# Performance work log

Hardware: AMD Instinct MI355X
Metric: run time of the kernel (lower is better)

Reference implementation:

```python
import jax, jax.numpy as jnp
import numpy as np

B = 8192          # batch
D = 256           # feature_dim
H = 64            # num attention heads
HD = D // H       # head_dim = 4
NC, NB, NF, NT = 2048, 2048, 512, 768
NCLS = 26
EPS = 1e-5


def _linear_params(k, out_d, in_d):
    s = 1.0 / np.sqrt(in_d)
    kw, kb = jax.random.split(k)
    W = jax.random.uniform(kw, (out_d, in_d), minval=-s, maxval=s, dtype=jnp.float32)
    b = jax.random.uniform(kb, (out_d,), minval=-s, maxval=s, dtype=jnp.float32)
    return W, b


def setup_inputs() -> dict:
    key = jax.random.key(0)
    ks = jax.random.split(key, 16)
    inp = {
        'x_context': jax.random.normal(ks[0], (B, NC), dtype=jnp.float32),
        'x_body':    jax.random.normal(ks[1], (B, NB), dtype=jnp.float32),
        'x_face':    jax.random.normal(ks[2], (B, NF), dtype=jnp.float32),
        'x_text':    jax.random.normal(ks[3], (B, NT), dtype=jnp.float32),
    }
    inp['Wc'], inp['bc'] = _linear_params(ks[4], D, NC)
    inp['Wb'], inp['bb'] = _linear_params(ks[5], D, NB)
    inp['Wf'], inp['bf'] = _linear_params(ks[6], D, NF)
    inp['Wt'], inp['bt'] = _linear_params(ks[7], D, NT)
    # MultiheadAttention packed in-proj (3D x D) and out-proj
    inp['in_w'], inp['in_b'] = _linear_params(ks[8], 3 * D, D)
    inp['out_w'], inp['out_b'] = _linear_params(ks[9], D, D)
    # gate MLP
    inp['Wg1'], inp['bg1'] = _linear_params(ks[10], D, D)
    inp['Wg2'], inp['bg2'] = _linear_params(ks[11], 1, D)
    # fusion head
    inp['W1'], inp['b1'] = _linear_params(ks[12], D, 4 * D)
    inp['gamma'] = jnp.ones((D,), dtype=jnp.float32)
    inp['beta'] = jnp.zeros((D,), dtype=jnp.float32)
    inp['W2'], inp['b2'] = _linear_params(ks[13], NCLS, D)
    return inp


def reference(x_context, x_body, x_face, x_text,
              Wc, bc, Wb, bb, Wf, bf, Wt, bt,
              in_w, in_b, out_w, out_b,
              Wg1, bg1, Wg2, bg2,
              W1, b1, gamma, beta, W2, b2):
    # per-modality projections -> [B, 4, D]
    f = jnp.stack([
        x_context @ Wc.T + bc,
        x_body    @ Wb.T + bb,
        x_face    @ Wf.T + bf,
        x_text    @ Wt.T + bt,
    ], axis=1)
    bsz = f.shape[0]

    # MultiheadAttention with seq_len=1 per token: softmax over a single key
    Wq, Wk, Wv = jnp.split(in_w, 3, axis=0)
    bq, bk, bv = jnp.split(in_b, 3)
    q = (f @ Wq.T + bq).reshape(bsz, 4, H, HD)
    k = (f @ Wk.T + bk).reshape(bsz, 4, H, HD)
    v = (f @ Wv.T + bv).reshape(bsz, 4, H, HD)
    scores = jnp.sum(q * k, axis=-1, keepdims=True) / np.sqrt(HD)  # [B,4,H,1]
    w = jax.nn.softmax(scores, axis=-1)                            # == 1 (single key)
    attn = (w * v).reshape(bsz, 4, D)
    self_out = attn @ out_w.T + out_b                              # [B,4,D]

    # cross attention: with seq_len=1 the output depends only on key/value,
    # so each (query i, key 3-j) call equals the self-style output of modality 3-j;
    # combining over the 4 key variants reduces to the mean over modalities.
    cross = jnp.mean(self_out, axis=1, keepdims=True)              # [B,1,D]

    gate = jax.nn.sigmoid(jax.nn.relu(self_out @ Wg1.T + bg1) @ Wg2.T + bg2)  # [B,4,1]
    combined = gate * self_out + (1.0 - gate) * cross              # [B,4,D]

    h = combined.reshape(bsz, 4 * D) @ W1.T + b1                   # [B,D]
    # BatchNorm1d (training-mode batch statistics, biased variance)
    mu = jnp.mean(h, axis=0)
    var = jnp.var(h, axis=0)
    h = (h - mu) / jnp.sqrt(var + EPS) * gamma + beta
    h = jax.nn.relu(h)                                             # dropout = identity (eval)
    return h @ W2.T + b2                                           # [B,26]
```

## Files before the change

kernel.cpp:

```cpp
#include <hip/hip_runtime.h>
#include <math.h>

typedef __attribute__((ext_vector_type(8))) short bf16x8;
typedef __attribute__((ext_vector_type(4))) float f32x4;
typedef unsigned short u16;
typedef unsigned int u32;

#define BSZ   8192
#define BN_EPS 1e-5f

__device__ inline u16 f2bf(float x) {
    u32 u = __float_as_uint(x);
    u32 r = (u + 0x7FFFu + ((u >> 16) & 1u)) >> 16;
    return (u16)r;
}
__device__ inline float bf2f_lo(u32 p) { return __uint_as_float(p << 16); }
__device__ inline float bf2f_hi(u32 p) { return __uint_as_float(p & 0xFFFF0000u); }

__device__ inline void async_g2l(const void* g, void* l) {
    __builtin_amdgcn_global_load_lds(
        (const __attribute__((address_space(1))) void*)g,
        (__attribute__((address_space(3))) void*)l, 16, 0, 0);
}

__global__ __launch_bounds__(256)
void wvo_kernel(const float* __restrict__ in_w, const float* __restrict__ in_b,
                const float* __restrict__ out_w, const float* __restrict__ out_b,
                float* __restrict__ wvo, float* __restrict__ bvo)
{
    const int i = blockIdx.x;
    const int j = threadIdx.x;
    const float* Wv = in_w + 512 * 256;
    float s = 0.f;
    for (int k = 0; k < 256; ++k)
        s = fmaf(out_w[i * 256 + k], Wv[k * 256 + j], s);
    wvo[i * 256 + j] = s;
    if (i == 0) {
        const float* bv = in_b + 512;
        float t = 0.f;
        for (int k = 0; k < 256; ++k)
            t = fmaf(out_w[j * 256 + k], bv[k], t);
        bvo[j] = t + out_b[j];
    }
}

__global__ __launch_bounds__(256)
void cvt_weights(const float* __restrict__ wvo, const float* __restrict__ Wc,
                 const float* __restrict__ Wb,  const float* __restrict__ Wf,
                 const float* __restrict__ Wt,  const float* __restrict__ Wg1,
                 const float* __restrict__ W1f, u16* __restrict__ dst)
{
    int gid = blockIdx.x * 256 + threadIdx.x;
    const float* src; u16* d; int loc;
    if      (gid <   8192) { src = wvo; d = dst + 0;       loc = gid; }
    else if (gid <  73728) { src = Wc;  d = dst + 65536;   loc = gid - 8192; }
    else if (gid < 139264) { src = Wb;  d = dst + 589824;  loc = gid - 73728; }
    else if (gid < 155648) { src = Wf;  d = dst + 1114112; loc = gid - 139264; }
    else if (gid < 180224) { src = Wt;  d = dst + 1245184; loc = gid - 155648; }
    else if (gid < 188416) { src = Wg1; d = dst + 1441792; loc = gid - 180224; }
    else                   { src = W1f; d = dst + 1507328; loc = gid - 188416; }
    const float4 v0 = *(const float4*)(src + (size_t)loc * 8);
    const float4 v1 = *(const float4*)(src + (size_t)loc * 8 + 4);
    uint4 o;
    o.x = (u32)f2bf(v0.x) | ((u32)f2bf(v0.y) << 16);
    o.y = (u32)f2bf(v0.z) | ((u32)f2bf(v0.w) << 16);
    o.z = (u32)f2bf(v1.x) | ((u32)f2bf(v1.y) << 16);
    o.w = (u32)f2bf(v1.z) | ((u32)f2bf(v1.w) << 16);
    *(uint4*)(d + (size_t)loc * 8) = o;
}

template<int ASRC, int EPI>
__device__ void gemm_core(const void* Ap, const u16* __restrict__ Wp,
                          const float* __restrict__ bias,
                          u16* __restrict__ outb, float* __restrict__ outf,
                          const float* __restrict__ wg2, float* __restrict__ gpart,
                          int K, int RMUL, int ROFF, int bm)
{
    __shared__ u16 As[64 * 64];
    __shared__ u16 Bs[256 * 64];
    const int t = threadIdx.x;
    const int w = t >> 6, l = t & 63;

    f32x4 acc[4][4];
    const f32x4 z = {0.f, 0.f, 0.f, 0.f};
#pragma unroll
    for (int i = 0; i < 4; ++i)
#pragma unroll
        for (int j = 0; j < 4; ++j) acc[i][j] = z;

    for (int k0 = 0; k0 < K; k0 += 64) {
#pragma unroll
        for (int it = 0; it < 8; ++it) {
            const int n  = it * 32 + w * 8 + (l >> 3);
            const int ch = (l & 7) ^ (n & 7);
            async_g2l(Wp + (size_t)n * K + k0 + ch * 8, Bs + it * 2048 + w * 512);
        }
        if (ASRC == 0) {
            const u16* Ab = (const u16*)Ap;
#pragma unroll
            for (int it = 0; it < 2; ++it) {
                const int row = it * 32 + w * 8 + (l >> 3);
                const int ch  = (l & 7) ^ (row & 7);
                async_g2l(Ab + (size_t)(bm + row) * K + k0 + ch * 8,
                          As + it * 2048 + w * 512);
            }
        } else {
            const float* Af = (const float*)Ap;
            const int row = t >> 2, kq = t & 3;
            const float* g = Af + (size_t)(bm + row) * K + k0 + kq * 16;
            const float4 v0 = *(const float4*)(g + 0);
            const float4 v1 = *(const float4*)(g + 4);
            const float4 v2 = *(const float4*)(g + 8);
            const float4 v3 = *(const float4*)(g + 12);
            bf16x8 p0, p1;
            p0[0] = (short)f2bf(v0.x); p0[1] = (short)f2bf(v0.y);
            p0[2] = (short)f2bf(v0.z); p0[3] = (short)f2bf(v0.w);
            p0[4] = (short)f2bf(v1.x); p0[5] = (short)f2bf(v1.y);
            p0[6] = (short)f2bf(v1.z); p0[7] = (short)f2bf(v1.w);
            p1[0] = (short)f2bf(v2.x); p1[1] = (short)f2bf(v2.y);
            p1[2] = (short)f2bf(v2.z); p1[3] = (short)f2bf(v2.w);
            p1[4] = (short)f2bf(v3.x); p1[5] = (short)f2bf(v3.y);
            p1[6] = (short)f2bf(v3.z); p1[7] = (short)f2bf(v3.w);
            char* ab = (char*)As;
            *(bf16x8*)(ab + row * 128 + (((kq * 2 + 0) ^ (row & 7)) << 4)) = p0;
            *(bf16x8*)(ab + row * 128 + (((kq * 2 + 1) ^ (row & 7)) << 4)) = p1;
        }
        __syncthreads();
        const char* ab = (const char*)As;
        const char* bb = (const char*)Bs;
#pragma unroll
        for (int kk = 0; kk < 2; ++kk) {
            bf16x8 af[4], bq[4];
#pragma unroll
            for (int i = 0; i < 4; ++i) {
                const int row = i * 16 + (l & 15);
                const int ch  = (l >> 4) + kk * 4;
                af[i] = *(const bf16x8*)(ab + row * 128 + ((ch ^ (row & 7)) << 4));
            }
#pragma unroll
            for (int j = 0; j < 4; ++j) {
                const int n  = w * 64 + j * 16 + (l & 15);
                const int ch = (l >> 4) + kk * 4;
                bq[j] = *(const bf16x8*)(bb + n * 128 + ((ch ^ (n & 7)) << 4));
            }
#pragma unroll
            for (int i = 0; i < 4; ++i)
#pragma unroll
                for (int j = 0; j < 4; ++j)
                    acc[i][j] = __builtin_amdgcn_mfma_f32_16x16x32_bf16(
                        af[i], bq[j], acc[i][j], 0, 0, 0);
        }
        __syncthreads();
    }

    if (EPI == 2) {
        float s[4][4];
#pragma unroll
        for (int i = 0; i < 4; ++i)
#pragma unroll
            for (int r = 0; r < 4; ++r) s[i][r] = 0.f;
#pragma unroll
        for (int j = 0; j < 4; ++j) {
            const int col = w * 64 + j * 16 + (l & 15);
            const float bv = bias[col], wv = wg2[col];
#pragma unroll
            for (int i = 0; i < 4; ++i)
#pragma unroll
                for (int r = 0; r < 4; ++r)
                    s[i][r] += fmaxf(acc[i][j][r] + bv, 0.f) * wv;
        }
#pragma unroll
        for (int off = 1; off < 16; off <<= 1)
#pragma unroll
            for (int i = 0; i < 4; ++i)
#pragma unroll
                for (int r = 0; r < 4; ++r)
                    s[i][r] += __shfl_xor(s[i][r], off);
        if ((l & 15) == 0) {
#pragma unroll
            for (int i = 0; i < 4; ++i)
#pragma unroll
                for (int r = 0; r < 4; ++r)
                    gpart[(size_t)w * 32768 + bm + i * 16 + ((l >> 4) << 2) + r] = s[i][r];
        }
    } else {
#pragma unroll
        for (int j = 0; j < 4; ++j) {
            const int col = w * 64 + j * 16 + (l & 15);
            const float bv = bias[col];
#pragma unroll
            for (int i = 0; i < 4; ++i) {
#pragma unroll
                for (int r = 0; r < 4; ++r) {
                    const int rt = i * 16 + ((l >> 4) << 2) + r;
                    const float v = acc[i][j][r] + bv;
                    const size_t orow = (size_t)(bm + rt) * RMUL + ROFF;
                    if (EPI == 0) outb[orow * 256 + col] = f2bf(v);
                    else          outf[orow * 256 + col] = v;
                }
            }
        }
    }
}

template<int ASRC, int EPI>
__global__ __launch_bounds__(256)
void gemm_k(const void* Ap, const u16* __restrict__ Wp, const float* __restrict__ bias,
            u16* __restrict__ outb, float* __restrict__ outf,
            const float* __restrict__ wg2, float* __restrict__ gpart, int K)
{
    gemm_core<ASRC, EPI>(Ap, Wp, bias, outb, outf, wg2, gpart, K, 1, 0, blockIdx.x * 64);
}

__global__ __launch_bounds__(256)
void gemm_proj(const float* A0, const float* A1, const float* A2, const float* A3,
               const u16* Wp0, const u16* Wp1, const u16* Wp2, const u16* Wp3,
               const float* b0, const float* b1, const float* b2, const float* b3,
               u16* __restrict__ fb)
{
    const int m = blockIdx.y;
    const float* A = (m == 0) ? A0 : (m == 1) ? A1 : (m == 2) ? A2 : A3;
    const u16* W   = (m == 0) ? Wp0 : (m == 1) ? Wp1 : (m == 2) ? Wp2 : Wp3;
    const float* b = (m == 0) ? b0 : (m == 1) ? b1 : (m == 2) ? b2 : b3;
    const int K    = (m == 0) ? 2048 : (m == 1) ? 2048 : (m == 2) ? 512 : 768;
    gemm_core<1, 0>(A, W, b, fb, nullptr, nullptr, nullptr, K, 4, m, blockIdx.x * 64);
}

__global__ __launch_bounds__(256)
void gate_fin(const float* __restrict__ gp, const float* __restrict__ bg2,
              float* __restrict__ gate)
{
    const int r = blockIdx.x * 256 + threadIdx.x;
    const float v = gp[r] + gp[32768 + r] + gp[65536 + r] + gp[98304 + r] + bg2[0];
    gate[r] = 1.f / (1.f + expf(-v));
}

__global__ __launch_bounds__(256)
void combined_k(const u16* __restrict__ so, const float* __restrict__ gate,
                u16* __restrict__ comb)
{
    const int idx = blockIdx.x * 256 + threadIdx.x;
    const int b = idx >> 7, p = idx & 127;
    const u32* s32 = (const u32*)so;
    u32* c32 = (u32*)comb;
    float lo[4], hi[4], gv[4];
#pragma unroll
    for (int m = 0; m < 4; ++m) {
        const u32 pk = s32[(size_t)(b * 4 + m) * 128 + p];
        lo[m] = bf2f_lo(pk); hi[m] = bf2f_hi(pk);
        gv[m] = gate[b * 4 + m];
    }
    const float cl = 0.25f * (lo[0] + lo[1] + lo[2] + lo[3]);
    const float ch = 0.25f * (hi[0] + hi[1] + hi[2] + hi[3]);
#pragma unroll
    for (int m = 0; m < 4; ++m) {
        const float ol = gv[m] * lo[m] + (1.f - gv[m]) * cl;
        const float oh = gv[m] * hi[m] + (1.f - gv[m]) * ch;
        c32[(size_t)b * 512 + m * 128 + p] = (u32)f2bf(ol) | ((u32)f2bf(oh) << 16);
    }
}

__global__ __launch_bounds__(256)
void bn_part(const float* __restrict__ h, float* __restrict__ psum,
             float* __restrict__ psq)
{
    const int p = blockIdx.x;
    const int d = threadIdx.x;
    float s = 0.f, q = 0.f;
    for (int r = 0; r < 128; ++r) {
        const float v = h[((size_t)p * 128 + r) * 256 + d];
        s += v;
        q = fmaf(v, v, q);
    }
    psum[p * 256 + d] = s;
    psq[p * 256 + d]  = q;
}

__global__ __launch_bounds__(256)
void bn_fin(const float* __restrict__ psum, const float* __restrict__ psq,
            const float* __restrict__ gamma, const float* __restrict__ beta,
            float* __restrict__ scale, float* __restrict__ shift)
{
    const int d = threadIdx.x;
    float s = 0.f, q = 0.f;
    for (int p = 0; p < 64; ++p) { s += psum[p * 256 + d]; q += psq[p * 256 + d]; }
    const float mu  = s * (1.f / BSZ);
    const float var = q * (1.f / BSZ) - mu * mu;
    const float inv = rsqrtf(var + BN_EPS);
    const float sc  = gamma[d] * inv;
    scale[d] = sc;
    shift[d] = beta[d] - mu * sc;
}

__global__ __launch_bounds__(256)
void final_kernel(const float* __restrict__ h, const float* __restrict__ scale,
                  const float* __restrict__ shift, const float* __restrict__ W2,
                  const float* __restrict__ b2, float* __restrict__ out)
{
    __shared__ float W2s[26][260];
    __shared__ float scs[256], shs[256];
    const int t = threadIdx.x;
    for (int u = t; u < 26 * 256; u += 256) {
        const int c = u >> 8, n = u & 255;
        W2s[c][(n >> 6) * 65 + (n & 63)] = W2[u];
    }
    scs[t] = scale[t];
    shs[t] = shift[t];
    __syncthreads();

    const int r = blockIdx.x * 64 + (t >> 2);
    const int p = t & 3;
    float acc[26];
#pragma unroll
    for (int c = 0; c < 26; ++c) acc[c] = 0.f;
    const float* hr = h + (size_t)r * 256 + p * 64;
#pragma unroll 4
    for (int i = 0; i < 64; ++i) {
        const int n = p * 64 + i;
        const float v = fmaxf(fmaf(hr[i], scs[n], shs[n]), 0.f);
        const int sw = p * 65 + i;
#pragma unroll
        for (int c = 0; c < 26; ++c)
            acc[c] = fmaf(v, W2s[c][sw], acc[c]);
    }
#pragma unroll
    for (int off = 1; off < 4; off <<= 1)
#pragma unroll
        for (int c = 0; c < 26; ++c)
            acc[c] += __shfl_xor(acc[c], off);
    if (p == 0) {
#pragma unroll
        for (int c = 0; c < 26; ++c)
            out[(size_t)r * 26 + c] = acc[c] + b2[c];
    }
}

extern "C" void kernel_launch(void* const* d_in, const int* in_sizes, int n_in,
                              void* d_out, int out_size, void* d_ws, size_t ws_size,
                              hipStream_t stream)
{
    const float* x_ctx  = (const float*)d_in[0];
    const float* x_body = (const float*)d_in[1];
    const float* x_face = (const float*)d_in[2];
    const float* x_text = (const float*)d_in[3];
    const float* Wc = (const float*)d_in[4];  const float* bc = (const float*)d_in[5];
    const float* Wb = (const float*)d_in[6];  const float* bb = (const float*)d_in[7];
    const float* Wf = (const float*)d_in[8];  const float* bf = (const float*)d_in[9];
    const float* Wt = (const float*)d_in[10]; const float* bt = (const float*)d_in[11];
    const float* in_w  = (const float*)d_in[12]; const float* in_b  = (const float*)d_in[13];
    const float* out_w = (const float*)d_in[14]; const float* out_b = (const float*)d_in[15];
    const float* Wg1 = (const float*)d_in[16]; const float* bg1 = (const float*)d_in[17];
    const float* Wg2 = (const float*)d_in[18]; const float* bg2 = (const float*)d_in[19];
    const float* W1  = (const float*)d_in[20]; const float* b1  = (const float*)d_in[21];
    const float* gamma = (const float*)d_in[22]; const float* beta = (const float*)d_in[23];
    const float* W2  = (const float*)d_in[24]; const float* b2  = (const float*)d_in[25];

    char* wsb = (char*)d_ws;
    u16*   f_bf  = (u16*)(wsb + 0);
    u16*   comb  = f_bf;
    u16*   so_bf = (u16*)(wsb + (16u << 20));
    float* h     = (float*)(wsb + (16u << 20));
    u16*   wpb   = (u16*)(wsb + (32u << 20));
    float* wvo   = (float*)(wsb + (36u << 20));
    float* bvo   = (float*)(wsb + (36u << 20) + 262144);
    float* gpart = (float*)(wsb + (37u << 20));
    float* gate  = (float*)(wsb + (38u << 20));
    float* psum  = (float*)(wsb + (39u << 20));
    float* psq   = (float*)(wsb + (39u << 20) + 65536);
    float* scale = (float*)(wsb + (39u << 20) + 131072);
    float* shift = (float*)(wsb + (39u << 20) + 135168);

    u16* wvo_bf = wpb + 0;
    u16* wc_bf  = wpb + 65536;
    u16* wb_bf  = wpb + 589824;
    u16* wf_bf  = wpb + 1114112;
    u16* wt_bf  = wpb + 1245184;
    u16* wg1_bf = wpb + 1441792;
    u16* w1_bf  = wpb + 1507328;

    wvo_kernel<<<256, 256, 0, stream>>>(in_w, in_b, out_w, out_b, wvo, bvo);
    cvt_weights<<<864, 256, 0, stream>>>(wvo, Wc, Wb, Wf, Wt, Wg1, W1, wpb);

    gemm_proj<<<dim3(128, 4), 256, 0, stream>>>(x_ctx, x_body, x_face, x_text,
                                                wc_bf, wb_bf, wf_bf, wt_bf,
                                                bc, bb, bf, bt, f_bf);

    gemm_k<0, 0><<<512, 256, 0, stream>>>(f_bf, wvo_bf, bvo, so_bf, nullptr,
                                          nullptr, nullptr, 256);

    gemm_k<0, 2><<<512, 256, 0, stream>>>(so_bf, wg1_bf, bg1, nullptr, nullptr,
                                          Wg2, gpart, 256);
    gate_fin<<<128, 256, 0, stream>>>(gpart, bg2, gate);

    combined_k<<<4096, 256, 0, stream>>>(so_bf, gate, comb);

    gemm_k<0, 1><<<128, 256, 0, stream>>>(comb, w1_bf, b1, nullptr, h,
                                          nullptr, nullptr, 1024);

    bn_part<<<64, 256, 0, stream>>>(h, psum, psq);
    bn_fin<<<1, 256, 0, stream>>>(psum, psq, gamma, beta, scale, shift);
    final_kernel<<<128, 256, 0, stream>>>(h, scale, shift, W2, b2, (float*)d_out);
}
```

Before: 166.1 us.

## Fuse self-out, gate MLP, combine and W1 GEMMs into one kernel; double-buffer projection GEMM

```diff
diff --git a/kernel.cpp b/kernel.cpp
--- a/kernel.cpp
+++ b/kernel.cpp
@@ -32,6 +32,7 @@
     const int j = threadIdx.x;
     const float* Wv = in_w + 512 * 256;
     float s = 0.f;
+#pragma unroll 8
     for (int k = 0; k < 256; ++k)
         s = fmaf(out_w[i * 256 + k], Wv[k * 256 + j], s);
     wvo[i * 256 + j] = s;
@@ -69,79 +70,90 @@
     *(uint4*)(d + (size_t)loc * 8) = o;
 }
 
-template<int ASRC, int EPI>
-__device__ void gemm_core(const void* Ap, const u16* __restrict__ Wp,
-                          const float* __restrict__ bias,
-                          u16* __restrict__ outb, float* __restrict__ outf,
-                          const float* __restrict__ wg2, float* __restrict__ gpart,
-                          int K, int RMUL, int ROFF, int bm)
-{
-    __shared__ u16 As[64 * 64];
-    __shared__ u16 Bs[256 * 64];
+__global__ __launch_bounds__(256)
+void gemm_proj(const float* __restrict__ A0, const float* __restrict__ A1,
+               const float* __restrict__ A2, const float* __restrict__ A3,
+               const u16* __restrict__ Wp0, const u16* __restrict__ Wp1,
+               const u16* __restrict__ Wp2, const u16* __restrict__ Wp3,
+               const float* __restrict__ b0, const float* __restrict__ b1,
+               const float* __restrict__ b2, const float* __restrict__ b3,
+               u16* __restrict__ fb)
+{
+    __shared__ u16 As[2][4096];
+    __shared__ u16 Bs[2][16384];
+    const int m = blockIdx.y;
+    const float* A  = (m == 0) ? A0 : (m == 1) ? A1 : (m == 2) ? A2 : A3;
+    const u16* Wp   = (m == 0) ? Wp0 : (m == 1) ? Wp1 : (m == 2) ? Wp2 : Wp3;
+    const float* bi = (m == 0) ? b0 : (m == 1) ? b1 : (m == 2) ? b2 : b3;
+    const int K     = (m == 0) ? 2048 : (m == 1) ? 2048 : (m == 2) ? 512 : 768;
+    const int nt = K >> 6;
+
     const int t = threadIdx.x;
     const int w = t >> 6, l = t & 63;
-
-    f32x4 acc[4][4];
-    const f32x4 z = {0.f, 0.f, 0.f, 0.f};
-#pragma unroll
-    for (int i = 0; i < 4; ++i)
-#pragma unroll
-        for (int j = 0; j < 4; ++j) acc[i][j] = z;
-
-    for (int k0 = 0; k0 < K; k0 += 64) {
+    const int bm = blockIdx.x * 64;
+    const int arow = t >> 2, akq = t & 3;
+
+    float4 ar[4];
+    auto loadA = [&](int k0) {
+        const float* g = A + (size_t)(bm + arow) * K + k0 + akq * 16;
+        ar[0] = *(const float4*)(g + 0);
+        ar[1] = *(const float4*)(g + 4);
+        ar[2] = *(const float4*)(g + 8);
+        ar[3] = *(const float4*)(g + 12);
+    };
+    auto writeA = [&](int buf) {
+        bf16x8 p0, p1;
+        p0[0] = (short)f2bf(ar[0].x); p0[1] = (short)f2bf(ar[0].y);
+        p0[2] = (short)f2bf(ar[0].z); p0[3] = (short)f2bf(ar[0].w);
+        p0[4] = (short)f2bf(ar[1].x); p0[5] = (short)f2bf(ar[1].y);
+        p0[6] = (short)f2bf(ar[1].z); p0[7] = (short)f2bf(ar[1].w);
+        p1[0] = (short)f2bf(ar[2].x); p1[1] = (short)f2bf(ar[2].y);
+        p1[2] = (short)f2bf(ar[2].z); p1[3] = (short)f2bf(ar[2].w);
+        p1[4] = (short)f2bf(ar[3].x); p1[5] = (short)f2bf(ar[3].y);
+        p1[6] = (short)f2bf(ar[3].z); p1[7] = (short)f2bf(ar[3].w);
+        char* abw = (char*)As[buf];
+        *(bf16x8*)(abw + arow * 128 + (((akq * 2 + 0) ^ (arow & 7)) << 4)) = p0;
+        *(bf16x8*)(abw + arow * 128 + (((akq * 2 + 1) ^ (arow & 7)) << 4)) = p1;
+    };
+    auto issueB = [&](int k0, int buf) {
 #pragma unroll
         for (int it = 0; it < 8; ++it) {
             const int n  = it * 32 + w * 8 + (l >> 3);
             const int ch = (l & 7) ^ (n & 7);
-            async_g2l(Wp + (size_t)n * K + k0 + ch * 8, Bs + it * 2048 + w * 512);
-        }
-        if (ASRC == 0) {
-            const u16* Ab = (const u16*)Ap;
-#pragma unroll
-            for (int it = 0; it < 2; ++it) {
-                const int row = it * 32 + w * 8 + (l >> 3);
-                const int ch  = (l & 7) ^ (row & 7);
-                async_g2l(Ab + (size_t)(bm + row) * K + k0 + ch * 8,
-                          As + it * 2048 + w * 512);
-            }
-        } else {
-            const float* Af = (const float*)Ap;
-            const int row = t >> 2, kq = t & 3;
-            const float* g = Af + (size_t)(bm + row) * K + k0 + kq * 16;
-            const float4 v0 = *(const float4*)(g + 0);
-            const float4 v1 = *(const float4*)(g + 4);
-            const float4 v2 = *(const float4*)(g + 8);
-            const float4 v3 = *(const float4*)(g + 12);
-            bf16x8 p0, p1;
-            p0[0] = (short)f2bf(v0.x); p0[1] = (short)f2bf(v0.y);
-            p0[2] = (short)f2bf(v0.z); p0[3] = (short)f2bf(v0.w);
-            p0[4] = (short)f2bf(v1.x); p0[5] = (short)f2bf(v1.y);
-            p0[6] = (short)f2bf(v1.z); p0[7] = (short)f2bf(v1.w);
-            p1[0] = (short)f2bf(v2.x); p1[1] = (short)f2bf(v2.y);
-            p1[2] = (short)f2bf(v2.z); p1[3] = (short)f2bf(v2.w);
-            p1[4] = (short)f2bf(v3.x); p1[5] = (short)f2bf(v3.y);
-            p1[6] = (short)f2bf(v3.z); p1[7] = (short)f2bf(v3.w);
-            char* ab = (char*)As;
-            *(bf16x8*)(ab + row * 128 + (((kq * 2 + 0) ^ (row & 7)) << 4)) = p0;
-            *(bf16x8*)(ab + row * 128 + (((kq * 2 + 1) ^ (row & 7)) << 4)) = p1;
-        }
-        __syncthreads();
-        const char* ab = (const char*)As;
-        const char* bb = (const char*)Bs;
+            async_g2l(Wp + (size_t)n * K + k0 + ch * 8, Bs[buf] + it * 2048 + w * 512);
+        }
+    };
+
+    f32x4 acc[4][4];
+    const f32x4 z = {0.f, 0.f, 0.f, 0.f};
+#pragma unroll
+    for (int i = 0; i < 4; ++i)
+#pragma unroll
+        for (int j = 0; j < 4; ++j) acc[i][j] = z;
+
+    loadA(0);
+    issueB(0, 0);
+    writeA(0);
+    __syncthreads();
+
+    for (int t0 = 0; t0 < nt; ++t0) {
+        const int cur = t0 & 1;
+        if (t0 + 1 < nt) { loadA((t0 + 1) * 64); issueB((t0 + 1) * 64, cur ^ 1); }
+        const char* abr = (const char*)As[cur];
+        const char* bbr = (const char*)Bs[cur];
 #pragma unroll
         for (int kk = 0; kk < 2; ++kk) {
             bf16x8 af[4], bq[4];
+            const int ch = kk * 4 + (l >> 4);
 #pragma unroll
             for (int i = 0; i < 4; ++i) {
-                const int row = i * 16 + (l & 15);
-                const int ch  = (l >> 4) + kk * 4;
-                af[i] = *(const bf16x8*)(ab + row * 128 + ((ch ^ (row & 7)) << 4));
+                const int fr = i * 16 + (l & 15);
+                af[i] = *(const bf16x8*)(abr + fr * 128 + ((ch ^ (fr & 7)) << 4));
             }
 #pragma unroll
             for (int j = 0; j < 4; ++j) {
-                const int n  = w * 64 + j * 16 + (l & 15);
-                const int ch = (l >> 4) + kk * 4;
-                bq[j] = *(const bf16x8*)(bb + n * 128 + ((ch ^ (n & 7)) << 4));
+                const int n = w * 64 + j * 16 + (l & 15);
+                bq[j] = *(const bf16x8*)(bbr + n * 128 + ((ch ^ (n & 7)) << 4));
             }
 #pragma unroll
             for (int i = 0; i < 4; ++i)
@@ -150,10 +162,157 @@
                     acc[i][j] = __builtin_amdgcn_mfma_f32_16x16x32_bf16(
                         af[i], bq[j], acc[i][j], 0, 0, 0);
         }
-        __syncthreads();
-    }
-
-    if (EPI == 2) {
+        if (t0 + 1 < nt) writeA(cur ^ 1);
+        __syncthreads();
+    }
+
+#pragma unroll
+    for (int j = 0; j < 4; ++j) {
+        const int col = w * 64 + j * 16 + (l & 15);
+        const float bv = bi[col];
+#pragma unroll
+        for (int i = 0; i < 4; ++i)
+#pragma unroll
+            for (int r = 0; r < 4; ++r) {
+                const int rt = i * 16 + ((l >> 4) << 2) + r;
+                fb[((size_t)(bm + rt) * 4 + m) * 256 + col] = f2bf(acc[i][j][r] + bv);
+            }
+    }
+}
+
+__global__ __launch_bounds__(256)
+void fused_mid(const u16* __restrict__ fb, const u16* __restrict__ wvo_bf,
+               const float* __restrict__ bvo,
+               const u16* __restrict__ wg1_bf, const float* __restrict__ bg1,
+               const float* __restrict__ wg2, const float* __restrict__ bg2,
+               const u16* __restrict__ w1_bf, const float* __restrict__ b1p,
+               float* __restrict__ h)
+{
+    __shared__ u16 AS[16384];
+    __shared__ u16 BS[16384];
+    __shared__ float gp[4][64];
+    __shared__ float gate[64];
+    const int t = threadIdx.x, w = t >> 6, l = t & 63;
+    const int bm = blockIdx.x * 64;
+    char* const ab = (char*)AS;
+    char* const bb = (char*)BS;
+
+    float4 br[8];
+    auto loadB = [&](const u16* Wp, int K, int k0) {
+#pragma unroll
+        for (int it = 0; it < 8; ++it) {
+            const int n  = it * 32 + w * 8 + (l >> 3);
+            const int ch = (l & 7) ^ (n & 7);
+            br[it] = *(const float4*)(Wp + (size_t)n * K + k0 + ch * 8);
+        }
+    };
+    auto writeB = [&]() {
+#pragma unroll
+        for (int it = 0; it < 8; ++it)
+            *(float4*)(bb + it * 4096 + w * 1024 + l * 16) = br[it];
+    };
+
+#pragma unroll
+    for (int it = 0; it < 8; ++it) {
+        const int r  = it * 8 + w * 2 + (l >> 5);
+        const int ch = l & 31;
+        async_g2l(fb + (size_t)(bm + r) * 256 + ((ch ^ (r & 7)) << 3),
+                  AS + it * 2048 + w * 512);
+    }
+    loadB(wvo_bf, 256, 0);
+    __syncthreads();
+
+    const f32x4 z = {0.f, 0.f, 0.f, 0.f};
+
+    f32x4 acc[4][4];
+#pragma unroll
+    for (int i = 0; i < 4; ++i)
+#pragma unroll
+        for (int j = 0; j < 4; ++j) acc[i][j] = z;
+
+    for (int it4 = 0; it4 < 4; ++it4) {
+        __syncthreads();
+        writeB();
+        if (it4 < 3) loadB(wvo_bf, 256, (it4 + 1) * 64);
+        __syncthreads();
+#pragma unroll
+        for (int kk = 0; kk < 2; ++kk) {
+            const int ks  = it4 * 2 + kk;
+            const int chB = kk * 4 + (l >> 4);
+            bf16x8 af[4], bq[4];
+#pragma unroll
+            for (int i = 0; i < 4; ++i) {
+                const int fr = i * 16 + (l & 15);
+                af[i] = *(const bf16x8*)(ab + fr * 512 +
+                          (((ks * 4 + (l >> 4)) ^ (fr & 7)) << 4));
+            }
+#pragma unroll
+            for (int j = 0; j < 4; ++j) {
+                const int n = w * 64 + j * 16 + (l & 15);
+                bq[j] = *(const bf16x8*)(bb + n * 128 + ((chB ^ (n & 7)) << 4));
+            }
+#pragma unroll
+            for (int i = 0; i < 4; ++i)
+#pragma unroll
+                for (int j = 0; j < 4; ++j)
+                    acc[i][j] = __builtin_amdgcn_mfma_f32_16x16x32_bf16(
+                        af[i], bq[j], acc[i][j], 0, 0, 0);
+        }
+    }
+
+    loadB(wg1_bf, 256, 0);
+    __syncthreads();
+#pragma unroll
+    for (int j = 0; j < 4; ++j) {
+        const int col = w * 64 + j * 16 + (l & 15);
+        const float bv = bvo[col];
+#pragma unroll
+        for (int i = 0; i < 4; ++i)
+#pragma unroll
+            for (int r = 0; r < 4; ++r) {
+                const int rt = i * 16 + ((l >> 4) << 2) + r;
+                *(u16*)(ab + rt * 512 + (((col >> 3) ^ (rt & 7)) << 4) + (col & 7) * 2)
+                    = f2bf(acc[i][j][r] + bv);
+            }
+    }
+
+    f32x4 g2[4][4];
+#pragma unroll
+    for (int i = 0; i < 4; ++i)
+#pragma unroll
+        for (int j = 0; j < 4; ++j) g2[i][j] = z;
+
+    for (int it4 = 0; it4 < 4; ++it4) {
+        __syncthreads();
+        writeB();
+        if (it4 < 3) loadB(wg1_bf, 256, (it4 + 1) * 64);
+        __syncthreads();
+#pragma unroll
+        for (int kk = 0; kk < 2; ++kk) {
+            const int ks  = it4 * 2 + kk;
+            const int chB = kk * 4 + (l >> 4);
+            bf16x8 af[4], bq[4];
+#pragma unroll
+            for (int i = 0; i < 4; ++i) {
+                const int fr = i * 16 + (l & 15);
+                af[i] = *(const bf16x8*)(ab + fr * 512 +
+                          (((ks * 4 + (l >> 4)) ^ (fr & 7)) << 4));
+            }
+#pragma unroll
+            for (int j = 0; j < 4; ++j) {
+                const int n = w * 64 + j * 16 + (l & 15);
+                bq[j] = *(const bf16x8*)(bb + n * 128 + ((chB ^ (n & 7)) << 4));
+            }
+#pragma unroll
+            for (int i = 0; i < 4; ++i)
+#pragma unroll
+                for (int j = 0; j < 4; ++j)
+                    g2[i][j] = __builtin_amdgcn_mfma_f32_16x16x32_bf16(
+                        af[i], bq[j], g2[i][j], 0, 0, 0);
+        }
+    }
+
+    {
         float s[4][4];
 #pragma unroll
         for (int i = 0; i < 4; ++i)
@@ -162,12 +321,12 @@
 #pragma unroll
         for (int j = 0; j < 4; ++j) {
             const int col = w * 64 + j * 16 + (l & 15);
-            const float bv = bias[col], wv = wg2[col];
+            const float bv = bg1[col], wv = wg2[col];
 #pragma unroll
             for (int i = 0; i < 4; ++i)
 #pragma unroll
                 for (int r = 0; r < 4; ++r)
-                    s[i][r] += fmaxf(acc[i][j][r] + bv, 0.f) * wv;
+                    s[i][r] += fmaxf(g2[i][j][r] + bv, 0.f) * wv;
         }
 #pragma unroll
         for (int off = 1; off < 16; off <<= 1)
@@ -181,82 +340,90 @@
             for (int i = 0; i < 4; ++i)
 #pragma unroll
                 for (int r = 0; r < 4; ++r)
-                    gpart[(size_t)w * 32768 + bm + i * 16 + ((l >> 4) << 2) + r] = s[i][r];
-        }
-    } else {
-#pragma unroll
-        for (int j = 0; j < 4; ++j) {
-            const int col = w * 64 + j * 16 + (l & 15);
-            const float bv = bias[col];
-#pragma unroll
-            for (int i = 0; i < 4; ++i) {
-#pragma unroll
-                for (int r = 0; r < 4; ++r) {
-                    const int rt = i * 16 + ((l >> 4) << 2) + r;
-                    const float v = acc[i][j][r] + bv;
-                    const size_t orow = (size_t)(bm + rt) * RMUL + ROFF;
-                    if (EPI == 0) outb[orow * 256 + col] = f2bf(v);
-                    else          outf[orow * 256 + col] = v;
-                }
-            }
-        }
-    }
-}
-
-template<int ASRC, int EPI>
-__global__ __launch_bounds__(256)
-void gemm_k(const void* Ap, const u16* __restrict__ Wp, const float* __restrict__ bias,
-            u16* __restrict__ outb, float* __restrict__ outf,
-            const float* __restrict__ wg2, float* __restrict__ gpart, int K)
-{
-    gemm_core<ASRC, EPI>(Ap, Wp, bias, outb, outf, wg2, gpart, K, 1, 0, blockIdx.x * 64);
-}
-
-__global__ __launch_bounds__(256)
-void gemm_proj(const float* A0, const float* A1, const float* A2, const float* A3,
-               const u16* Wp0, const u16* Wp1, const u16* Wp2, const u16* Wp3,
-               const float* b0, const float* b1, const float* b2, const float* b3,
-               u16* __restrict__ fb)
-{
-    const int m = blockIdx.y;
-    const float* A = (m == 0) ? A0 : (m == 1) ? A1 : (m == 2) ? A2 : A3;
-    const u16* W   = (m == 0) ? Wp0 : (m == 1) ? Wp1 : (m == 2) ? Wp2 : Wp3;
-    const float* b = (m == 0) ? b0 : (m == 1) ? b1 : (m == 2) ? b2 : b3;
-    const int K    = (m == 0) ? 2048 : (m == 1) ? 2048 : (m == 2) ? 512 : 768;
-    gemm_core<1, 0>(A, W, b, fb, nullptr, nullptr, nullptr, K, 4, m, blockIdx.x * 64);
-}
-
-__global__ __launch_bounds__(256)
-void gate_fin(const float* __restrict__ gp, const float* __restrict__ bg2,
-              float* __restrict__ gate)
-{
-    const int r = blockIdx.x * 256 + threadIdx.x;
-    const float v = gp[r] + gp[32768 + r] + gp[65536 + r] + gp[98304 + r] + bg2[0];
-    gate[r] = 1.f / (1.f + expf(-v));
-}
-
-__global__ __launch_bounds__(256)
-void combined_k(const u16* __restrict__ so, const float* __restrict__ gate,
-                u16* __restrict__ comb)
-{
-    const int idx = blockIdx.x * 256 + threadIdx.x;
-    const int b = idx >> 7, p = idx & 127;
-    const u32* s32 = (const u32*)so;
-    u32* c32 = (u32*)comb;
-    float lo[4], hi[4], gv[4];
-#pragma unroll
-    for (int m = 0; m < 4; ++m) {
-        const u32 pk = s32[(size_t)(b * 4 + m) * 128 + p];
-        lo[m] = bf2f_lo(pk); hi[m] = bf2f_hi(pk);
-        gv[m] = gate[b * 4 + m];
-    }
-    const float cl = 0.25f * (lo[0] + lo[1] + lo[2] + lo[3]);
-    const float ch = 0.25f * (hi[0] + hi[1] + hi[2] + hi[3]);
-#pragma unroll
-    for (int m = 0; m < 4; ++m) {
-        const float ol = gv[m] * lo[m] + (1.f - gv[m]) * cl;
-        const float oh = gv[m] * hi[m] + (1.f - gv[m]) * ch;
-        c32[(size_t)b * 512 + m * 128 + p] = (u32)f2bf(ol) | ((u32)f2bf(oh) << 16);
+                    gp[w][i * 16 + ((l >> 4) << 2) + r] = s[i][r];
+        }
+    }
+    loadB(w1_bf, 1024, 0);
+    __syncthreads();
+    if (t < 64) {
+        const float g = gp[0][t] + gp[1][t] + gp[2][t] + gp[3][t] + bg2[0];
+        gate[t] = 1.f / (1.f + expf(-g));
+    }
+    __syncthreads();
+
+#pragma unroll
+    for (int hf = 0; hf < 2; ++hf) {
+        const int d0  = hf * 128 + l * 2;
+        const int chh = d0 >> 3;
+        const int bo  = (d0 & 7) * 2;
+        float ol[4][4], oh[4][4];
+#pragma unroll
+        for (int s4 = 0; s4 < 4; ++s4) {
+            const int g = w * 4 + s4;
+            float lo4[4], hi4[4];
+#pragma unroll
+            for (int mm = 0; mm < 4; ++mm) {
+                const int fr = g * 4 + mm;
+                const u32 v = *(const u32*)(ab + fr * 512 + ((chh ^ (fr & 7)) << 4) + bo);
+                lo4[mm] = bf2f_lo(v); hi4[mm] = bf2f_hi(v);
+            }
+            const float cl = 0.25f * (lo4[0] + lo4[1] + lo4[2] + lo4[3]);
+            const float ch = 0.25f * (hi4[0] + hi4[1] + hi4[2] + hi4[3]);
+#pragma unroll
+            for (int mm = 0; mm < 4; ++mm) {
+                const float gv = gate[g * 4 + mm];
+                ol[s4][mm] = gv * lo4[mm] + (1.f - gv) * cl;
+                oh[s4][mm] = gv * hi4[mm] + (1.f - gv) * ch;
+            }
+        }
+        __syncthreads();
+#pragma unroll
+        for (int s4 = 0; s4 < 4; ++s4) {
+            const int r = w * 4 + s4;
+#pragma unroll
+            for (int mm = 0; mm < 4; ++mm) {
+                const int ch2 = mm * 32 + (d0 >> 3);
+                const u32 pk = (u32)f2bf(ol[s4][mm]) | ((u32)f2bf(oh[s4][mm]) << 16);
+                *(u32*)(ab + r * 2048 + ((ch2 ^ (r & 7)) << 4) + bo) = pk;
+            }
+        }
+        __syncthreads();
+    }
+
+    f32x4 a3[4];
+#pragma unroll
+    for (int j = 0; j < 4; ++j) a3[j] = z;
+
+    for (int it16 = 0; it16 < 16; ++it16) {
+        __syncthreads();
+        writeB();
+        if (it16 < 15) loadB(w1_bf, 1024, (it16 + 1) * 64);
+        __syncthreads();
+#pragma unroll
+        for (int kk = 0; kk < 2; ++kk) {
+            const int fr  = l & 15;
+            const int chA = it16 * 8 + kk * 4 + (l >> 4);
+            const int chB = kk * 4 + (l >> 4);
+            const bf16x8 afr = *(const bf16x8*)(ab + fr * 2048 + ((chA ^ (fr & 7)) << 4));
+#pragma unroll
+            for (int j = 0; j < 4; ++j) {
+                const int n = w * 64 + j * 16 + (l & 15);
+                const bf16x8 bq = *(const bf16x8*)(bb + n * 128 + ((chB ^ (n & 7)) << 4));
+                a3[j] = __builtin_amdgcn_mfma_f32_16x16x32_bf16(afr, bq, a3[j], 0, 0, 0);
+            }
+        }
+    }
+
+    const int base = blockIdx.x * 16;
+#pragma unroll
+    for (int j = 0; j < 4; ++j) {
+        const int col = w * 64 + j * 16 + (l & 15);
+        const float bv = b1p[col];
+#pragma unroll
+        for (int r = 0; r < 4; ++r) {
+            const int ht = ((l >> 4) << 2) + r;
+            h[(size_t)(base + ht) * 256 + col] = a3[j][r] + bv;
+        }
     }
 }
 
@@ -267,6 +434,7 @@
     const int p = blockIdx.x;
     const int d = threadIdx.x;
     float s = 0.f, q = 0.f;
+#pragma unroll 8
     for (int r = 0; r < 128; ++r) {
         const float v = h[((size_t)p * 128 + r) * 256 + d];
         s += v;
@@ -283,6 +451,7 @@
 {
     const int d = threadIdx.x;
     float s = 0.f, q = 0.f;
+#pragma unroll 8
     for (int p = 0; p < 64; ++p) { s += psum[p * 256 + d]; q += psq[p * 256 + d]; }
     const float mu  = s * (1.f / BSZ);
     const float var = q * (1.f / BSZ) - mu * mu;
@@ -357,18 +526,14 @@
 
     char* wsb = (char*)d_ws;
     u16*   f_bf  = (u16*)(wsb + 0);
-    u16*   comb  = f_bf;
-    u16*   so_bf = (u16*)(wsb + (16u << 20));
     float* h     = (float*)(wsb + (16u << 20));
     u16*   wpb   = (u16*)(wsb + (32u << 20));
     float* wvo   = (float*)(wsb + (36u << 20));
     float* bvo   = (float*)(wsb + (36u << 20) + 262144);
-    float* gpart = (float*)(wsb + (37u << 20));
-    float* gate  = (float*)(wsb + (38u << 20));
-    float* psum  = (float*)(wsb + (39u << 20));
-    float* psq   = (float*)(wsb + (39u << 20) + 65536);
-    float* scale = (float*)(wsb + (39u << 20) + 131072);
-    float* shift = (float*)(wsb + (39u << 20) + 135168);
+    float* psum  = (float*)(wsb + (37u << 20));
+    float* psq   = (float*)(wsb + (37u << 20) + 65536);
+    float* scale = (float*)(wsb + (37u << 20) + 131072);
+    float* shift = (float*)(wsb + (37u << 20) + 135168);
 
     u16* wvo_bf = wpb + 0;
     u16* wc_bf  = wpb + 65536;
@@ -385,17 +550,8 @@
                                                 wc_bf, wb_bf, wf_bf, wt_bf,
                                                 bc, bb, bf, bt, f_bf);
 
-    gemm_k<0, 0><<<512, 256, 0, stream>>>(f_bf, wvo_bf, bvo, so_bf, nullptr,
-                                          nullptr, nullptr, 256);
-
-    gemm_k<0, 2><<<512, 256, 0, stream>>>(so_bf, wg1_bf, bg1, nullptr, nullptr,
-                                          Wg2, gpart, 256);
-    gate_fin<<<128, 256, 0, stream>>>(gpart, bg2, gate);
-
-    combined_k<<<4096, 256, 0, stream>>>(so_bf, gate, comb);
-
-    gemm_k<0, 1><<<128, 256, 0, stream>>>(comb, w1_bf, b1, nullptr, h,
-                                          nullptr, nullptr, 1024);
+    fused_mid<<<512, 256, 0, stream>>>(f_bf, wvo_bf, bvo, wg1_bf, bg1,
+                                       Wg2, bg2, w1_bf, b1, h);
 
     bn_part<<<64, 256, 0, stream>>>(h, psum, psq);
     bn_fin<<<1, 256, 0, stream>>>(psum, psq, gamma, beta, scale, shift);
```

Result: slower. 219.6 us (+32.2%).

## Double-buffer GEMM tiles to overlap global loads with MFMA compute

Applied to the files above, without the earlier changes.

```diff
diff --git a/kernel.cpp b/kernel.cpp
--- a/kernel.cpp
+++ b/kernel.cpp
@@ -32,6 +32,7 @@
     const int j = threadIdx.x;
     const float* Wv = in_w + 512 * 256;
     float s = 0.f;
+#pragma unroll 8
     for (int k = 0; k < 256; ++k)
         s = fmaf(out_w[i * 256 + k], Wv[k * 256 + j], s);
     wvo[i * 256 + j] = s;
@@ -69,79 +70,90 @@
     *(uint4*)(d + (size_t)loc * 8) = o;
 }
 
-template<int ASRC, int EPI>
-__device__ void gemm_core(const void* Ap, const u16* __restrict__ Wp,
-                          const float* __restrict__ bias,
-                          u16* __restrict__ outb, float* __restrict__ outf,
-                          const float* __restrict__ wg2, float* __restrict__ gpart,
-                          int K, int RMUL, int ROFF, int bm)
-{
-    __shared__ u16 As[64 * 64];
-    __shared__ u16 Bs[256 * 64];
+__global__ __launch_bounds__(256)
+void gemm_proj(const float* __restrict__ A0, const float* __restrict__ A1,
+               const float* __restrict__ A2, const float* __restrict__ A3,
+               const u16* __restrict__ Wp0, const u16* __restrict__ Wp1,
+               const u16* __restrict__ Wp2, const u16* __restrict__ Wp3,
+               const float* __restrict__ b0, const float* __restrict__ b1,
+               const float* __restrict__ b2, const float* __restrict__ b3,
+               u16* __restrict__ fb)
+{
+    __shared__ u16 As[2][4096];
+    __shared__ u16 Bs[2][16384];
+    const int m = blockIdx.y;
+    const float* A  = (m == 0) ? A0 : (m == 1) ? A1 : (m == 2) ? A2 : A3;
+    const u16* Wp   = (m == 0) ? Wp0 : (m == 1) ? Wp1 : (m == 2) ? Wp2 : Wp3;
+    const float* bi = (m == 0) ? b0 : (m == 1) ? b1 : (m == 2) ? b2 : b3;
+    const int K     = (m == 0) ? 2048 : (m == 1) ? 2048 : (m == 2) ? 512 : 768;
+    const int nt = K >> 6;
+
     const int t = threadIdx.x;
     const int w = t >> 6, l = t & 63;
-
-    f32x4 acc[4][4];
-    const f32x4 z = {0.f, 0.f, 0.f, 0.f};
-#pragma unroll
-    for (int i = 0; i < 4; ++i)
-#pragma unroll
-        for (int j = 0; j < 4; ++j) acc[i][j] = z;
-
-    for (int k0 = 0; k0 < K; k0 += 64) {
+    const int bm = blockIdx.x * 64;
+    const int arow = t >> 2, akq = t & 3;
+
+    float4 ar[4];
+    auto loadA = [&](int k0) {
+        const float* g = A + (size_t)(bm + arow) * K + k0 + akq * 16;
+        ar[0] = *(const float4*)(g + 0);
+        ar[1] = *(const float4*)(g + 4);
+        ar[2] = *(const float4*)(g + 8);
+        ar[3] = *(const float4*)(g + 12);
+    };
+    auto writeA = [&](int buf) {
+        bf16x8 p0, p1;
+        p0[0] = (short)f2bf(ar[0].x); p0[1] = (short)f2bf(ar[0].y);
+        p0[2] = (short)f2bf(ar[0].z); p0[3] = (short)f2bf(ar[0].w);
+        p0[4] = (short)f2bf(ar[1].x); p0[5] = (short)f2bf(ar[1].y);
+        p0[6] = (short)f2bf(ar[1].z); p0[7] = (short)f2bf(ar[1].w);
+        p1[0] = (short)f2bf(ar[2].x); p1[1] = (short)f2bf(ar[2].y);
+        p1[2] = (short)f2bf(ar[2].z); p1[3] = (short)f2bf(ar[2].w);
+        p1[4] = (short)f2bf(ar[3].x); p1[5] = (short)f2bf(ar[3].y);
+        p1[6] = (short)f2bf(ar[3].z); p1[7] = (short)f2bf(ar[3].w);
+        char* abw = (char*)As[buf];
+        *(bf16x8*)(abw + arow * 128 + (((akq * 2 + 0) ^ (arow & 7)) << 4)) = p0;
+        *(bf16x8*)(abw + arow * 128 + (((akq * 2 + 1) ^ (arow & 7)) << 4)) = p1;
+    };
+    auto issueB = [&](int k0, int buf) {
 #pragma unroll
         for (int it = 0; it < 8; ++it) {
             const int n  = it * 32 + w * 8 + (l >> 3);
             const int ch = (l & 7) ^ (n & 7);
-            async_g2l(Wp + (size_t)n * K + k0 + ch * 8, Bs + it * 2048 + w * 512);
-        }
-        if (ASRC == 0) {
-            const u16* Ab = (const u16*)Ap;
-#pragma unroll
-            for (int it = 0; it < 2; ++it) {
-                const int row = it * 32 + w * 8 + (l >> 3);
-                const int ch  = (l & 7) ^ (row & 7);
-                async_g2l(Ab + (size_t)(bm + row) * K + k0 + ch * 8,
-                          As + it * 2048 + w * 512);
-            }
-        } else {
-            const float* Af = (const float*)Ap;
-            const int row = t >> 2, kq = t & 3;
-            const float* g = Af + (size_t)(bm + row) * K + k0 + kq * 16;
-            const float4 v0 = *(const float4*)(g + 0);
-            const float4 v1 = *(const float4*)(g + 4);
-            const float4 v2 = *(const float4*)(g + 8);
-            const float4 v3 = *(const float4*)(g + 12);
-            bf16x8 p0, p1;
-            p0[0] = (short)f2bf(v0.x); p0[1] = (short)f2bf(v0.y);
-            p0[2] = (short)f2bf(v0.z); p0[3] = (short)f2bf(v0.w);
-            p0[4] = (short)f2bf(v1.x); p0[5] = (short)f2bf(v1.y);
-            p0[6] = (short)f2bf(v1.z); p0[7] = (short)f2bf(v1.w);
-            p1[0] = (short)f2bf(v2.x); p1[1] = (short)f2bf(v2.y);
-            p1[2] = (short)f2bf(v2.z); p1[3] = (short)f2bf(v2.w);
-            p1[4] = (short)f2bf(v3.x); p1[5] = (short)f2bf(v3.y);
-            p1[6] = (short)f2bf(v3.z); p1[7] = (short)f2bf(v3.w);
-            char* ab = (char*)As;
-            *(bf16x8*)(ab + row * 128 + (((kq * 2 + 0) ^ (row & 7)) << 4)) = p0;
-            *(bf16x8*)(ab + row * 128 + (((kq * 2 + 1) ^ (row & 7)) << 4)) = p1;
-        }
-        __syncthreads();
-        const char* ab = (const char*)As;
-        const char* bb = (const char*)Bs;
+            async_g2l(Wp + (size_t)n * K + k0 + ch * 8, Bs[buf] + it * 2048 + w * 512);
+        }
+    };
+
+    f32x4 acc[4][4];
+    const f32x4 z = {0.f, 0.f, 0.f, 0.f};
+#pragma unroll
+    for (int i = 0; i < 4; ++i)
+#pragma unroll
+        for (int j = 0; j < 4; ++j) acc[i][j] = z;
+
+    loadA(0);
+    issueB(0, 0);
+    writeA(0);
+    __syncthreads();
+
+    for (int t0 = 0; t0 < nt; ++t0) {
+        const int cur = t0 & 1;
+        if (t0 + 1 < nt) { loadA((t0 + 1) * 64); issueB((t0 + 1) * 64, cur ^ 1); }
+        const char* abr = (const char*)As[cur];
+        const char* bbr = (const char*)Bs[cur];
 #pragma unroll
         for (int kk = 0; kk < 2; ++kk) {
             bf16x8 af[4], bq[4];
+            const int ch = kk * 4 + (l >> 4);
 #pragma unroll
             for (int i = 0; i < 4; ++i) {
-                const int row = i * 16 + (l & 15);
-                const int ch  = (l >> 4) + kk * 4;
-                af[i] = *(const bf16x8*)(ab + row * 128 + ((ch ^ (row & 7)) << 4));
+                const int fr = i * 16 + (l & 15);
+                af[i] = *(const bf16x8*)(abr + fr * 128 + ((ch ^ (fr & 7)) << 4));
             }
 #pragma unroll
             for (int j = 0; j < 4; ++j) {
-                const int n  = w * 64 + j * 16 + (l & 15);
-                const int ch = (l >> 4) + kk * 4;
-                bq[j] = *(const bf16x8*)(bb + n * 128 + ((ch ^ (n & 7)) << 4));
+                const int n = w * 64 + j * 16 + (l & 15);
+                bq[j] = *(const bf16x8*)(bbr + n * 128 + ((ch ^ (n & 7)) << 4));
             }
 #pragma unroll
             for (int i = 0; i < 4; ++i)
@@ -150,6 +162,90 @@
                     acc[i][j] = __builtin_amdgcn_mfma_f32_16x16x32_bf16(
                         af[i], bq[j], acc[i][j], 0, 0, 0);
         }
+        if (t0 + 1 < nt) writeA(cur ^ 1);
+        __syncthreads();
+    }
+
+#pragma unroll
+    for (int j = 0; j < 4; ++j) {
+        const int col = w * 64 + j * 16 + (l & 15);
+        const float bv = bi[col];
+#pragma unroll
+        for (int i = 0; i < 4; ++i)
+#pragma unroll
+            for (int r = 0; r < 4; ++r) {
+                const int rt = i * 16 + ((l >> 4) << 2) + r;
+                fb[((size_t)(bm + rt) * 4 + m) * 256 + col] = f2bf(acc[i][j][r] + bv);
+            }
+    }
+}
+
+template<int EPI>
+__global__ __launch_bounds__(256)
+void gemm_mid(const u16* __restrict__ Ab, const u16* __restrict__ Wp,
+              const float* __restrict__ bias,
+              u16* __restrict__ outb, float* __restrict__ outf,
+              const float* __restrict__ wg2, float* __restrict__ gpart, int K)
+{
+    __shared__ u16 As[2][4096];
+    __shared__ u16 Bs[2][16384];
+    const int t = threadIdx.x;
+    const int w = t >> 6, l = t & 63;
+    const int bm = blockIdx.x * 64;
+    const int nt = K >> 6;
+
+    auto issueAB = [&](int k0, int buf) {
+#pragma unroll
+        for (int it = 0; it < 8; ++it) {
+            const int n  = it * 32 + w * 8 + (l >> 3);
+            const int ch = (l & 7) ^ (n & 7);
+            async_g2l(Wp + (size_t)n * K + k0 + ch * 8, Bs[buf] + it * 2048 + w * 512);
+        }
+#pragma unroll
+        for (int it = 0; it < 2; ++it) {
+            const int row = it * 32 + w * 8 + (l >> 3);
+            const int ch  = (l & 7) ^ (row & 7);
+            async_g2l(Ab + (size_t)(bm + row) * K + k0 + ch * 8,
+                      As[buf] + it * 2048 + w * 512);
+        }
+    };
+
+    f32x4 acc[4][4];
+    const f32x4 z = {0.f, 0.f, 0.f, 0.f};
+#pragma unroll
+    for (int i = 0; i < 4; ++i)
+#pragma unroll
+        for (int j = 0; j < 4; ++j) acc[i][j] = z;
+
+    issueAB(0, 0);
+    __syncthreads();
+
+    for (int t0 = 0; t0 < nt; ++t0) {
+        const int cur = t0 & 1;
+        if (t0 + 1 < nt) issueAB((t0 + 1) * 64, cur ^ 1);
+        const char* abr = (const char*)As[cur];
+        const char* bbr = (const char*)Bs[cur];
+#pragma unroll
+        for (int kk = 0; kk < 2; ++kk) {
+            bf16x8 af[4], bq[4];
+            const int ch = kk * 4 + (l >> 4);
+#pragma unroll
+            for (int i = 0; i < 4; ++i) {
+                const int fr = i * 16 + (l & 15);
+                af[i] = *(const bf16x8*)(abr + fr * 128 + ((ch ^ (fr & 7)) << 4));
+            }
+#pragma unroll
+            for (int j = 0; j < 4; ++j) {
+                const int n = w * 64 + j * 16 + (l & 15);
+                bq[j] = *(const bf16x8*)(bbr + n * 128 + ((ch ^ (n & 7)) << 4));
+            }
+#pragma unroll
+            for (int i = 0; i < 4; ++i)
+#pragma unroll
+                for (int j = 0; j < 4; ++j)
+                    acc[i][j] = __builtin_amdgcn_mfma_f32_16x16x32_bf16(
+                        af[i], bq[j], acc[i][j], 0, 0, 0);
+        }
         __syncthreads();
     }
 
@@ -189,41 +285,16 @@
             const int col = w * 64 + j * 16 + (l & 15);
             const float bv = bias[col];
 #pragma unroll
-            for (int i = 0; i < 4; ++i) {
+            for (int i = 0; i < 4; ++i)
 #pragma unroll
                 for (int r = 0; r < 4; ++r) {
                     const int rt = i * 16 + ((l >> 4) << 2) + r;
                     const float v = acc[i][j][r] + bv;
-                    const size_t orow = (size_t)(bm + rt) * RMUL + ROFF;
-                    if (EPI == 0) outb[orow * 256 + col] = f2bf(v);
-                    else          outf[orow * 256 + col] = v;
+                    if (EPI == 0) outb[(size_t)(bm + rt) * 256 + col] = f2bf(v);
+                    else          outf[(size_t)(bm + rt) * 256 + col] = v;
                 }
-            }
-        }
-    }
-}
-
-template<int ASRC, int EPI>
-__global__ __launch_bounds__(256)
-void gemm_k(const void* Ap, const u16* __restrict__ Wp, const float* __restrict__ bias,
-            u16* __restrict__ outb, float* __restrict__ outf,
-            const float* __restrict__ wg2, float* __restrict__ gpart, int K)
-{
-    gemm_core<ASRC, EPI>(Ap, Wp, bias, outb, outf, wg2, gpart, K, 1, 0, blockIdx.x * 64);
-}
-
-__global__ __launch_bounds__(256)
-void gemm_proj(const float* A0, const float* A1, const float* A2, const float* A3,
-               const u16* Wp0, const u16* Wp1, const u16* Wp2, const u16* Wp3,
-               const float* b0, const float* b1, const float* b2, const float* b3,
-               u16* __restrict__ fb)
-{
-    const int m = blockIdx.y;
-    const float* A = (m == 0) ? A0 : (m == 1) ? A1 : (m == 2) ? A2 : A3;
-    const u16* W   = (m == 0) ? Wp0 : (m == 1) ? Wp1 : (m == 2) ? Wp2 : Wp3;
-    const float* b = (m == 0) ? b0 : (m == 1) ? b1 : (m == 2) ? b2 : b3;
-    const int K    = (m == 0) ? 2048 : (m == 1) ? 2048 : (m == 2) ? 512 : 768;
-    gemm_core<1, 0>(A, W, b, fb, nullptr, nullptr, nullptr, K, 4, m, blockIdx.x * 64);
+        }
+    }
 }
 
 __global__ __launch_bounds__(256)
@@ -267,8 +338,9 @@
     const int p = blockIdx.x;
     const int d = threadIdx.x;
     float s = 0.f, q = 0.f;
-    for (int r = 0; r < 128; ++r) {
-        const float v = h[((size_t)p * 128 + r) * 256 + d];
+#pragma unroll 8
+    for (int r = 0; r < 32; ++r) {
+        const float v = h[((size_t)p * 32 + r) * 256 + d];
         s += v;
         q = fmaf(v, v, q);
     }
@@ -283,7 +355,8 @@
 {
     const int d = threadIdx.x;
     float s = 0.f, q = 0.f;
-    for (int p = 0; p < 64; ++p) { s += psum[p * 256 + d]; q += psq[p * 256 + d]; }
+#pragma unroll 8
+    for (int p = 0; p < 256; ++p) { s += psum[p * 256 + d]; q += psq[p * 256 + d]; }
     const float mu  = s * (1.f / BSZ);
     const float var = q * (1.f / BSZ) - mu * mu;
     const float inv = rsqrtf(var + BN_EPS);
@@ -314,14 +387,20 @@
 #pragma unroll
     for (int c = 0; c < 26; ++c) acc[c] = 0.f;
     const float* hr = h + (size_t)r * 256 + p * 64;
-#pragma unroll 4
-    for (int i = 0; i < 64; ++i) {
-        const int n = p * 64 + i;
-        const float v = fmaxf(fmaf(hr[i], scs[n], shs[n]), 0.f);
-        const int sw = p * 65 + i;
-#pragma unroll
-        for (int c = 0; c < 26; ++c)
-            acc[c] = fmaf(v, W2s[c][sw], acc[c]);
+#pragma unroll
+    for (int i4 = 0; i4 < 16; ++i4) {
+        const float4 v4 = *(const float4*)(hr + i4 * 4);
+#pragma unroll
+        for (int q = 0; q < 4; ++q) {
+            const int i = i4 * 4 + q;
+            const int n = p * 64 + i;
+            const float vv = (q == 0) ? v4.x : (q == 1) ? v4.y : (q == 2) ? v4.z : v4.w;
+            const float v = fmaxf(fmaf(vv, scs[n], shs[n]), 0.f);
+            const int sw = p * 65 + i;
+#pragma unroll
+            for (int c = 0; c < 26; ++c)
+                acc[c] = fmaf(v, W2s[c][sw], acc[c]);
+        }
     }
 #pragma unroll
     for (int off = 1; off < 4; off <<= 1)
@@ -366,9 +445,9 @@
     float* gpart = (float*)(wsb + (37u << 20));
     float* gate  = (float*)(wsb + (38u << 20));
     float* psum  = (float*)(wsb + (39u << 20));
-    float* psq   = (float*)(wsb + (39u << 20) + 65536);
-    float* scale = (float*)(wsb + (39u << 20) + 131072);
-    float* shift = (float*)(wsb + (39u << 20) + 135168);
+    float* psq   = (float*)(wsb + (39u << 20) + 262144);
+    float* scale = (float*)(wsb + (39u << 20) + 524288);
+    float* shift = (float*)(wsb + (39u << 20) + 528384);
 
     u16* wvo_bf = wpb + 0;
     u16* wc_bf  = wpb + 65536;
@@ -385,19 +464,19 @@
                                                 wc_bf, wb_bf, wf_bf, wt_bf,
                                                 bc, bb, bf, bt, f_bf);
 
-    gemm_k<0, 0><<<512, 256, 0, stream>>>(f_bf, wvo_bf, bvo, so_bf, nullptr,
-                                          nullptr, nullptr, 256);
-
-    gemm_k<0, 2><<<512, 256, 0, stream>>>(so_bf, wg1_bf, bg1, nullptr, nullptr,
-                                          Wg2, gpart, 256);
+    gemm_mid<0><<<512, 256, 0, stream>>>(f_bf, wvo_bf, bvo, so_bf, nullptr,
+                                         nullptr, nullptr, 256);
+
+    gemm_mid<2><<<512, 256, 0, stream>>>(so_bf, wg1_bf, bg1, nullptr, nullptr,
+                                         Wg2, gpart, 256);
     gate_fin<<<128, 256, 0, stream>>>(gpart, bg2, gate);
 
     combined_k<<<4096, 256, 0, stream>>>(so_bf, gate, comb);
 
-    gemm_k<0, 1><<<128, 256, 0, stream>>>(comb, w1_bf, b1, nullptr, h,
-                                          nullptr, nullptr, 1024);
-
-    bn_part<<<64, 256, 0, stream>>>(h, psum, psq);
+    gemm_mid<1><<<128, 256, 0, stream>>>(comb, w1_bf, b1, nullptr, h,
+                                         nullptr, nullptr, 1024);
+
+    bn_part<<<256, 256, 0, stream>>>(h, psum, psq);
     bn_fin<<<1, 256, 0, stream>>>(psum, psq, gamma, beta, scale, shift);
     final_kernel<<<128, 256, 0, stream>>>(h, scale, shift, W2, b2, (float*)d_out);
 }
```

New measurement: 162.5 us. 1.02x faster.
